# Optimization experiments

Measured on AMD Instinct MI355X. Metric: run time of the kernel, lower is better.

Reference implementation:

```python
import jax, jax.numpy as jnp
import numpy as np
from jax import lax

EPS = 1e-5
K_UP = 5
RATIO = 2
PAD = 2


def conv1x1(x, w):
    # x: (B,C,H,W), w: (O,C)
    return jnp.einsum('bchw,oc->bohw', x, w)


def bn(x, g, b, m, v):
    inv = g / jnp.sqrt(v + EPS)
    return x * inv[None, :, None, None] + (b - m * inv)[None, :, None, None]


def relu6(x):
    return jnp.clip(x, 0.0, 6.0)


def carafe_down(x, wc, bc, we, be):
    # content-aware reassembly kernels
    y = conv1x1(x, wc) + bc[None, :, None, None]              # (B, 64, H, W)
    y = lax.conv_general_dilated(
        y, we, window_strides=(RATIO, RATIO), padding=[(PAD, PAD), (PAD, PAD)],
        dimension_numbers=('NCHW', 'OIHW', 'NCHW')) + be[None, :, None, None]
    w = jax.nn.softmax(y, axis=1)                              # (B, 25, Ho, Wo)
    B, C, H, W = x.shape
    Ho, Wo = H // RATIO, W // RATIO
    xp = jnp.pad(x, ((0, 0), (0, 0), (PAD, PAD), (PAD, PAD)))
    out = jnp.zeros((B, C, Ho, Wo), x.dtype)
    k = 0
    for i in range(K_UP):
        for j in range(K_UP):
            patch = xp[:, :, i:i + RATIO * Ho:RATIO, j:j + RATIO * Wo:RATIO]
            out = out + patch * w[:, k][:, None]
            k += 1
    return out


def setup_inputs() -> dict:
    key = jax.random.key(0)
    ks = jax.random.split(key, 20)
    B, INP, H, W = 8, 64, 112, 112
    OUP, HID, CMID = 128, 384, 64

    def bn_params(k, c):
        k1, k2, k3, k4 = jax.random.split(k, 4)
        return (jax.random.uniform(k1, (c,), jnp.float32, 0.5, 1.5),
                jax.random.normal(k2, (c,), jnp.float32) * 0.1,
                jax.random.normal(k3, (c,), jnp.float32) * 0.1,
                jax.random.uniform(k4, (c,), jnp.float32, 0.5, 1.5))
    g1, b1, m1, v1 = bn_params(ks[1], HID)
    g2, b2, m2, v2 = bn_params(ks[2], HID)
    g3, b3, m3, v3 = bn_params(ks[3], OUP)
    return {
        'x': jax.random.normal(ks[0], (B, INP, H, W), jnp.float32),
        'w1': jax.random.normal(ks[4], (HID, INP), jnp.float32) / np.sqrt(INP),
        'g1': g1, 'b1': b1, 'm1': m1, 'v1': v1,
        'wc': jax.random.normal(ks[5], (CMID, HID), jnp.float32) / np.sqrt(HID),
        'bc': jax.random.normal(ks[6], (CMID,), jnp.float32) * 0.01,
        'we': jax.random.normal(ks[7], (K_UP**2, CMID, 5, 5), jnp.float32) / np.sqrt(CMID * 25),
        'be': jax.random.normal(ks[8], (K_UP**2,), jnp.float32) * 0.01,
        'g2': g2, 'b2': b2, 'm2': m2, 'v2': v2,
        'w2': jax.random.normal(ks[9], (OUP, HID), jnp.float32) / np.sqrt(HID),
        'g3': g3, 'b3': b3, 'm3': m3, 'v3': v3,
    }


def reference(x, w1, g1, b1, m1, v1, wc, bc, we, be, g2, b2, m2, v2, w2, g3, b3, m3, v3):
    # stride-2 InvertedResidualBlockCarafe (no identity): 1x1 expand -> BN -> ReLU6
    # -> CARAFE_downsample -> BN -> ReLU6 -> 1x1 project -> BN
    h = relu6(bn(conv1x1(x, w1), g1, b1, m1, v1))
    h = relu6(bn(carafe_down(h, wc, bc, we, be), g2, b2, m2, v2))
    return bn(conv1x1(h, w2), g3, b3, m3, v3)
```

## Files before the change

### kernel.cpp

```cpp
#include <hip/hip_runtime.h>
#include <hip/hip_bf16.h>
#include <type_traits>

#define EPS 1e-5f

typedef _Float16 half8 __attribute__((ext_vector_type(8)));
typedef _Float16 half4 __attribute__((ext_vector_type(4)));
typedef _Float16 half2v __attribute__((ext_vector_type(2)));
typedef float f32x4 __attribute__((ext_vector_type(4)));

__global__ __launch_bounds__(256) void fold_k(
    const float* __restrict__ w1, const float* __restrict__ g1, const float* __restrict__ b1,
    const float* __restrict__ m1, const float* __restrict__ v1,
    const float* __restrict__ wc,
    const float* __restrict__ g2, const float* __restrict__ b2,
    const float* __restrict__ m2, const float* __restrict__ v2,
    const float* __restrict__ w2, const float* __restrict__ g3, const float* __restrict__ b3,
    const float* __restrict__ m3, const float* __restrict__ v3,
    _Float16* __restrict__ w1h, float* __restrict__ bias1,
    _Float16* __restrict__ wch,
    _Float16* __restrict__ w2h, float* __restrict__ bias3,
    float* __restrict__ s2, float* __restrict__ t2) {
  int i = blockIdx.x * 256 + threadIdx.x;
  if (i < 384 * 64) {
    int o = i >> 6;
    float inv = g1[o] / sqrtf(v1[o] + EPS);
    w1h[i] = (_Float16)(w1[i] * inv);
  }
  if (i < 64 * 384) wch[i] = (_Float16)wc[i];
  if (i < 128 * 384) {
    int o = i / 384;
    float inv = g3[o] / sqrtf(v3[o] + EPS);
    w2h[i] = (_Float16)(w2[i] * inv);
  }
  if (i < 384) {
    float inv = g1[i] / sqrtf(v1[i] + EPS);
    bias1[i] = b1[i] - m1[i] * inv;
    float inv2 = g2[i] / sqrtf(v2[i] + EPS);
    s2[i] = inv2;
    t2[i] = b2[i] - m2[i] * inv2;
  }
  if (i < 128) {
    float inv = g3[i] / sqrtf(v3[i] + EPS);
    bias3[i] = b3[i] - m3[i] * inv;
  }
}

__global__ __launch_bounds__(256) void wtrans2_k(const float* __restrict__ we,
                                                 _Float16* __restrict__ wa) {
  int i = blockIdx.x * 256 + threadIdx.x;
  if (i >= 51200) return;
  int j = i & 7;
  int lane = (i >> 3) & 63;
  int f = i >> 9;
  int ocf = f & 1;
  int tap = (f >> 1) % 25;
  int ph = f / 50;
  int oc = ocf * 16 + (lane & 15);
  int cm = ph * 32 + (lane >> 4) * 8 + j;
  float v = (oc < 25) ? we[((size_t)oc * 64 + cm) * 25 + tap] : 0.f;
  wa[i] = (_Float16)v;
}

template <int IC, int NPF, int ACT, typename TI, typename TO>
__global__ __launch_bounds__(256) void gemm16_k(
    const TI* __restrict__ in, const _Float16* __restrict__ wh,
    const float* __restrict__ bias, TO* __restrict__ out, int npx) {
  constexpr int BPX = NPF * 64;
  constexpr int L2B = (BPX == 128) ? 7 : 6;
  constexpr int PAD = 16 / sizeof(TO);
  constexpr int CH = 16 / sizeof(TO);
  constexpr int SPAN = NPF * 16;
  constexpr int LPO = SPAN / CH;
  constexpr int OCPI = 64 / LPO;
  using vec16 = std::conditional_t<std::is_same_v<TO, _Float16>, half8, float4>;

  __shared__ _Float16 xh[BPX][40];
  __shared__ TO oT[64][BPX + PAD];

  const int tid = threadIdx.x;
  const int lane = tid & 63;
  const int w = tid >> 6;
  const int l15 = lane & 15;
  const int g = lane >> 4;
  const int wpx = w * SPAN;
  const int oc0 = blockIdx.x * 64;
  const int p0 = blockIdx.y * BPX;
  const int b = blockIdx.z;
  const int OCT = gridDim.x * 64;
  const TI* inb = in + (size_t)b * IC * npx + p0;

  f32x4 acc[4][NPF];
#pragma unroll
  for (int fo = 0; fo < 4; ++fo)
#pragma unroll
    for (int pf = 0; pf < NPF; ++pf)
      acc[fo][pf] = (f32x4){0.f, 0.f, 0.f, 0.f};

  for (int kk = 0; kk < IC; kk += 32) {
    __syncthreads();
    half8 a[4];
#pragma unroll
    for (int fo = 0; fo < 4; ++fo)
      a[fo] = *(const half8*)&wh[(size_t)(oc0 + fo * 16 + l15) * IC + kk + g * 8];
#pragma unroll
    for (int i = 0; i < NPF * 2; ++i) {
      int slot = tid + 256 * i;
      int px = slot & (BPX - 1);
      int kq = slot >> L2B;
      const TI* src = inb + (size_t)(kk + kq * 4) * npx + px;
      half4 v = {(_Float16)src[0], (_Float16)src[npx],
                 (_Float16)src[2 * npx], (_Float16)src[3 * npx]};
      *(half4*)&xh[px][kq * 4] = v;
    }
    __syncthreads();
    half8 xb[NPF];
#pragma unroll
    for (int pf = 0; pf < NPF; ++pf)
      xb[pf] = *(const half8*)&xh[wpx + pf * 16 + l15][g * 8];
#pragma unroll
    for (int fo = 0; fo < 4; ++fo)
#pragma unroll
      for (int pf = 0; pf < NPF; ++pf)
        acc[fo][pf] = __builtin_amdgcn_mfma_f32_16x16x32_f16(
            a[fo], xb[pf], acc[fo][pf], 0, 0, 0);
  }

#pragma unroll
  for (int fo = 0; fo < 4; ++fo) {
#pragma unroll
    for (int r = 0; r < 4; ++r) {
      float bz = bias[oc0 + fo * 16 + g * 4 + r];
#pragma unroll
      for (int pf = 0; pf < NPF; ++pf) {
        float v = acc[fo][pf][r] + bz;
        if (ACT) v = fminf(fmaxf(v, 0.f), 6.f);
        oT[fo * 16 + g * 4 + r][wpx + pf * 16 + l15] = (TO)v;
      }
    }
  }
#pragma unroll
  for (int i = 0; i < LPO; ++i) {
    int oc = i * OCPI + lane / LPO;
    int pxo = (lane % LPO) * CH;
    vec16 v = *(const vec16*)&oT[oc][wpx + pxo];
    *(vec16*)&out[((size_t)b * OCT + oc0 + oc) * npx + p0 + wpx + pxo] = v;
  }
}

__global__ __launch_bounds__(256) void mask_conv5_k(
    const _Float16* __restrict__ y, const _Float16* __restrict__ wa,
    float* __restrict__ lg) {
  __shared__ _Float16 ysh[32][5][136];
  const int ho = blockIdx.x;
  const int b = blockIdx.y;
  const int tid = threadIdx.x;
  const int lane = tid & 63;
  const int w = tid >> 6;
  const int l15 = lane & 15;
  const int g = lane >> 4;
  const int wo = w * 16 + l15;
  const int woe = (wo < 56) ? wo : 55;
  const int ci0 = 2 * woe + 6;

  for (int i = tid; i < 640; i += 256) {
    int ch = i / 20; int rem = i - ch * 20; int ri = rem / 4; int q = rem & 3;
    *(uint*)&ysh[ch][ri][q * 2] = 0u;
  }
  for (int i = tid; i < 1280; i += 256) {
    int ch = i / 40; int rem = i - ch * 40; int ri = rem / 8; int q = rem & 7;
    *(uint*)&ysh[ch][ri][120 + q * 2] = 0u;
  }

  f32x4 acc[2] = {(f32x4){0.f, 0.f, 0.f, 0.f}, (f32x4){0.f, 0.f, 0.f, 0.f}};

  for (int ph = 0; ph < 2; ++ph) {
    __syncthreads();
    for (int i = tid; i < 2240; i += 256) {
      int ch = i / 70;
      int rem = i - ch * 70;
      int ri = rem / 14;
      int j8 = rem - ri * 14;
      int hi = 2 * ho - 2 + ri;
      half8 v = {0, 0, 0, 0, 0, 0, 0, 0};
      if ((unsigned)hi < 112u)
        v = *(const half8*)&y[((size_t)(b * 64 + ph * 32 + ch) * 112 + hi) * 112 + j8 * 8];
      *(half8*)&ysh[ch][ri][8 + j8 * 8] = v;
    }
    __syncthreads();

    const _Float16* wap = wa + (size_t)ph * 25600;
#pragma unroll
    for (int di = 0; di < 5; ++di) {
      half2v pa[8], pb[8];
      _Float16 pc[8];
#pragma unroll
      for (int j = 0; j < 8; ++j) {
        pa[j] = *(const half2v*)&ysh[g * 8 + j][di][ci0];
        pb[j] = *(const half2v*)&ysh[g * 8 + j][di][ci0 + 2];
        pc[j] = ysh[g * 8 + j][di][ci0 + 4];
      }
#pragma unroll
      for (int dj = 0; dj < 5; ++dj) {
        half8 bf;
#pragma unroll
        for (int j = 0; j < 8; ++j)
          bf[j] = (dj == 0) ? pa[j][0]
                : (dj == 1) ? pa[j][1]
                : (dj == 2) ? pb[j][0]
                : (dj == 3) ? pb[j][1]
                            : pc[j];
        const int tap = di * 5 + dj;
        half8 a0 = *(const half8*)&wap[(tap * 2 + 0) * 512 + lane * 8];
        half8 a1 = *(const half8*)&wap[(tap * 2 + 1) * 512 + lane * 8];
        acc[0] = __builtin_amdgcn_mfma_f32_16x16x32_f16(a0, bf, acc[0], 0, 0, 0);
        acc[1] = __builtin_amdgcn_mfma_f32_16x16x32_f16(a1, bf, acc[1], 0, 0, 0);
      }
    }
  }

  if (wo < 56) {
#pragma unroll
    for (int ocf = 0; ocf < 2; ++ocf)
#pragma unroll
      for (int r = 0; r < 4; ++r) {
        int oc = ocf * 16 + g * 4 + r;
        if (oc < 25)
          lg[((size_t)b * 25 + oc) * 3136 + ho * 56 + wo] = acc[ocf][r];
      }
  }
}

__global__ __launch_bounds__(256) void softmax3_k(
    const float* __restrict__ lg, const float* __restrict__ be,
    float* __restrict__ msk) {
  int idx = blockIdx.x * 256 + threadIdx.x;
  if (idx >= 8 * 3136) return;
  int b = idx / 3136, sp = idx - (idx / 3136) * 3136;
  float v[25];
  float mx = -1e30f;
#pragma unroll
  for (int k = 0; k < 25; ++k) {
    float s = lg[((size_t)b * 25 + k) * 3136 + sp] + be[k];
    v[k] = s;
    mx = fmaxf(mx, s);
  }
  float s = 0.f;
#pragma unroll
  for (int k = 0; k < 25; ++k) {
    v[k] = __expf(v[k] - mx);
    s += v[k];
  }
  float inv = 1.0f / s;
#pragma unroll
  for (int k = 0; k < 25; ++k)
    msk[((size_t)b * 25 + k) * 3136 + sp] = v[k] * inv;
}

__device__ __forceinline__ void stage_pair(float dst[2][19][120],
                                           const _Float16* __restrict__ hbase,
                                           int ho0, int tid) {
  for (int i = tid; i < 2 * 19 * 14; i += 512) {
    int ch = i / 266;
    int rem = i - ch * 266;
    int rr = rem / 14;
    int j8 = rem - rr * 14;
    int hi = 2 * ho0 - 2 + rr;
    float4 lo = {0.f, 0.f, 0.f, 0.f}, hi4 = {0.f, 0.f, 0.f, 0.f};
    if ((unsigned)hi < 112u) {
      half8 v = *(const half8*)&hbase[(size_t)ch * 12544 + hi * 112 + j8 * 8];
      lo = (float4){(float)v[0], (float)v[1], (float)v[2], (float)v[3]};
      hi4 = (float4){(float)v[4], (float)v[5], (float)v[6], (float)v[7]};
    }
    *(float4*)&dst[ch][rr][4 + j8 * 8] = lo;
    *(float4*)&dst[ch][rr][8 + j8 * 8] = hi4;
  }
}

__global__ __launch_bounds__(512) void carafe3_k(
    const _Float16* __restrict__ h, const float* __restrict__ msk,
    const float* __restrict__ s2, const float* __restrict__ t2,
    _Float16* __restrict__ h2) {
  __shared__ float ys[2][2][19][120];
  const int hx = blockIdx.x;
  const int b  = blockIdx.y;
  const int cz = blockIdx.z;
  const int ho0 = hx * 8;
  const int tid = threadIdx.x;
  const int r = tid / 56;
  const int c = tid - r * 56;
  const int c0 = cz * 24;

  for (int i = tid; i < 2 * 2 * 19 * 8; i += 512) {
    int bufi = i / 304;
    int rem = i - bufi * 304;
    int ch = rem / 152;
    int rem2 = rem - ch * 152;
    int rr = rem2 / 8;
    int p = rem2 - rr * 8;
    int col = (p < 4) ? p : (112 + p);
    ys[bufi][ch][rr][col] = 0.f;
  }

  float m[25];
  if (tid < 448) {
    const float* mp = msk + (size_t)b * 25 * 3136 + (ho0 + r) * 56 + c;
#pragma unroll
    for (int k = 0; k < 25; ++k) m[k] = mp[(size_t)k * 3136];
  }
  __syncthreads();

  stage_pair(ys[0], h + (size_t)(b * 384 + c0) * 12544, ho0, tid);
  __syncthreads();

#pragma unroll
  for (int p = 0; p < 12; ++p) {
    const int bf = p & 1;
    if (p + 1 < 12)
      stage_pair(ys[bf ^ 1], h + (size_t)(b * 384 + c0 + 2 * (p + 1)) * 12544,
                 ho0, tid);
    if (tid < 448) {
#pragma unroll
      for (int cl = 0; cl < 2; ++cl) {
        const int cc = c0 + 2 * p + cl;
        float acc = 0.f;
#pragma unroll
        for (int di = 0; di < 5; ++di) {
          const float* row = &ys[bf][cl][2 * r + di][2 * c + 2];
          float2 a01 = *(const float2*)&row[0];
          float2 a23 = *(const float2*)&row[2];
          float a4 = row[4];
          acc = fmaf(a01.x, m[di * 5 + 0], acc);
          acc = fmaf(a01.y, m[di * 5 + 1], acc);
          acc = fmaf(a23.x, m[di * 5 + 2], acc);
          acc = fmaf(a23.y, m[di * 5 + 3], acc);
          acc = fmaf(a4,    m[di * 5 + 4], acc);
        }
        float o = s2[cc] * acc + t2[cc];
        h2[((size_t)(b * 384 + cc) * 56 + ho0 + r) * 56 + c] =
            (_Float16)fminf(fmaxf(o, 0.f), 6.f);
      }
    }
    __syncthreads();
  }
}

extern "C" void kernel_launch(void* const* d_in, const int* in_sizes, int n_in,
                              void* d_out, int out_size, void* d_ws, size_t ws_size,
                              hipStream_t stream) {
  const float* x  = (const float*)d_in[0];
  const float* w1 = (const float*)d_in[1];
  const float* g1 = (const float*)d_in[2];
  const float* b1 = (const float*)d_in[3];
  const float* m1 = (const float*)d_in[4];
  const float* v1 = (const float*)d_in[5];
  const float* wc = (const float*)d_in[6];
  const float* bc = (const float*)d_in[7];
  const float* we = (const float*)d_in[8];
  const float* be = (const float*)d_in[9];
  const float* g2 = (const float*)d_in[10];
  const float* b2 = (const float*)d_in[11];
  const float* m2 = (const float*)d_in[12];
  const float* v2 = (const float*)d_in[13];
  const float* w2 = (const float*)d_in[14];
  const float* g3 = (const float*)d_in[15];
  const float* b3 = (const float*)d_in[16];
  const float* m3 = (const float*)d_in[17];
  const float* v3 = (const float*)d_in[18];
  float* out = (float*)d_out;

  _Float16* hq  = (_Float16*)d_ws;
  _Float16* yq  = hq + 38535168;
  _Float16* h2q = yq + 6422528;
  float* lg     = (float*)(h2q + 9633792);
  float* mskf   = lg + 627200;
  float* bias1  = mskf + 627200;
  float* bias3  = bias1 + 384;
  float* s2     = bias3 + 128;
  float* t2     = s2 + 384;
  _Float16* w1h = (_Float16*)(t2 + 384);
  _Float16* wch = w1h + 24576;
  _Float16* w2h = wch + 24576;
  _Float16* wa  = w2h + 49152;

  fold_k<<<192, 256, 0, stream>>>(w1, g1, b1, m1, v1, wc, g2, b2, m2, v2,
                                  w2, g3, b3, m3, v3,
                                  w1h, bias1, wch, w2h, bias3, s2, t2);
  wtrans2_k<<<200, 256, 0, stream>>>(we, wa);

  gemm16_k<64, 2, 1, float, _Float16>
      <<<dim3(6, 98, 8), 256, 0, stream>>>(x, w1h, bias1, hq, 12544);

  gemm16_k<384, 2, 0, _Float16, _Float16>
      <<<dim3(1, 98, 8), 256, 0, stream>>>(hq, wch, bc, yq, 12544);

  mask_conv5_k<<<dim3(56, 8), 256, 0, stream>>>(yq, wa, lg);
  softmax3_k<<<98, 256, 0, stream>>>(lg, be, mskf);

  carafe3_k<<<dim3(7, 8, 16), 512, 0, stream>>>(hq, mskf, s2, t2, h2q);

  gemm16_k<384, 1, 0, _Float16, float>
      <<<dim3(2, 49, 8), 256, 0, stream>>>(h2q, w2h, bias3, out, 3136);
}
```

Baseline: 162.5 us.

## Fuse expand GEMM and CARAFE compressor GEMM into one kernel

Adds a fused kernel that computes the 1x1 expand conv with BN and ReLU6 for all 384 channels of a 64-pixel tile, keeps the result in shared memory, and feeds it straight into the 384-to-64 compressor GEMM. The separate re-read of the 384-channel fp16 intermediate from global memory for the second GEMM goes away. The intermediate is still written out for the later CARAFE stage. The kernel uses about 62KB of LDS and 96 accumulator VGPRs per thread, which may limit occupancy. The grid axes of the generic GEMM are also swapped so that pixel tiles come first.

```diff
diff --git a/kernel.cpp b/kernel.cpp
--- a/kernel.cpp
+++ b/kernel.cpp
@@ -62,6 +62,105 @@
   wa[i] = (_Float16)v;
 }
 
+__global__ __launch_bounds__(256) void fused1_k(
+    const float* __restrict__ x, const _Float16* __restrict__ w1h,
+    const float* __restrict__ bias1, const _Float16* __restrict__ wch,
+    const float* __restrict__ bc, _Float16* __restrict__ hq,
+    _Float16* __restrict__ yq) {
+  __shared__ __align__(16) unsigned char smem_raw[63488];
+  _Float16 (*xh)[40]  = (_Float16 (*)[40])smem_raw;
+  _Float16 (*hT)[76]  = (_Float16 (*)[76])(smem_raw + 5120);
+  _Float16 (*oTy)[72] = (_Float16 (*)[72])(smem_raw + 5120);
+
+  const int tid = threadIdx.x;
+  const int lane = tid & 63;
+  const int w = tid >> 6;
+  const int l15 = lane & 15;
+  const int g = lane >> 4;
+  const int wpx = w * 16;
+  const int p0 = blockIdx.x * 64;
+  const int b = blockIdx.y;
+  const float* inb = x + (size_t)b * 64 * 12544 + p0;
+
+  f32x4 acc1[24];
+#pragma unroll
+  for (int fo = 0; fo < 24; ++fo) acc1[fo] = (f32x4){0.f, 0.f, 0.f, 0.f};
+
+  for (int kk = 0; kk < 64; kk += 32) {
+    __syncthreads();
+#pragma unroll
+    for (int i = 0; i < 2; ++i) {
+      int slot = tid + 256 * i;
+      int px = slot & 63;
+      int kq = slot >> 6;
+      const float* src = inb + (size_t)(kk + kq * 4) * 12544 + px;
+      half4 v = {(_Float16)src[0], (_Float16)src[12544],
+                 (_Float16)src[2 * 12544], (_Float16)src[3 * 12544]};
+      *(half4*)&xh[px][kq * 4] = v;
+    }
+    __syncthreads();
+    half8 xb = *(const half8*)&xh[wpx + l15][g * 8];
+#pragma unroll
+    for (int fo = 0; fo < 24; ++fo) {
+      half8 a = *(const half8*)&w1h[(size_t)(fo * 16 + l15) * 64 + kk + g * 8];
+      acc1[fo] = __builtin_amdgcn_mfma_f32_16x16x32_f16(a, xb, acc1[fo], 0, 0, 0);
+    }
+  }
+
+#pragma unroll
+  for (int fo = 0; fo < 24; ++fo) {
+#pragma unroll
+    for (int r = 0; r < 4; ++r) {
+      int oc = fo * 16 + g * 4 + r;
+      float v = acc1[fo][r] + bias1[oc];
+      v = fminf(fmaxf(v, 0.f), 6.f);
+      hT[oc][wpx + l15] = (_Float16)v;
+    }
+  }
+  __syncthreads();
+
+#pragma unroll
+  for (int i = 0; i < 12; ++i) {
+    int idx = tid + 256 * i;
+    int row = idx >> 3, j8 = idx & 7;
+    half8 v = *(const half8*)&hT[row][j8 * 8];
+    *(half8*)&hq[(size_t)(b * 384 + row) * 12544 + p0 + j8 * 8] = v;
+  }
+
+  f32x4 acc2[4];
+#pragma unroll
+  for (int fo2 = 0; fo2 < 4; ++fo2) acc2[fo2] = (f32x4){0.f, 0.f, 0.f, 0.f};
+#pragma unroll
+  for (int ks = 0; ks < 12; ++ks) {
+    half8 bf;
+#pragma unroll
+    for (int j = 0; j < 8; ++j) bf[j] = hT[ks * 32 + g * 8 + j][wpx + l15];
+#pragma unroll
+    for (int fo2 = 0; fo2 < 4; ++fo2) {
+      half8 a = *(const half8*)&wch[(size_t)(fo2 * 16 + l15) * 384 + ks * 32 + g * 8];
+      acc2[fo2] = __builtin_amdgcn_mfma_f32_16x16x32_f16(a, bf, acc2[fo2], 0, 0, 0);
+    }
+  }
+  __syncthreads();
+
+#pragma unroll
+  for (int fo2 = 0; fo2 < 4; ++fo2) {
+#pragma unroll
+    for (int r = 0; r < 4; ++r) {
+      int oc2 = fo2 * 16 + g * 4 + r;
+      oTy[oc2][wpx + l15] = (_Float16)(acc2[fo2][r] + bc[oc2]);
+    }
+  }
+  __syncthreads();
+#pragma unroll
+  for (int i = 0; i < 2; ++i) {
+    int slot = tid + 256 * i;
+    int row = slot >> 3, j8 = slot & 7;
+    half8 v = *(const half8*)&oTy[row][j8 * 8];
+    *(half8*)&yq[(size_t)(b * 64 + row) * 12544 + p0 + j8 * 8] = v;
+  }
+}
+
 template <int IC, int NPF, int ACT, typename TI, typename TO>
 __global__ __launch_bounds__(256) void gemm16_k(
     const TI* __restrict__ in, const _Float16* __restrict__ wh,
@@ -84,10 +183,10 @@
   const int l15 = lane & 15;
   const int g = lane >> 4;
   const int wpx = w * SPAN;
-  const int oc0 = blockIdx.x * 64;
-  const int p0 = blockIdx.y * BPX;
+  const int p0 = blockIdx.x * BPX;
+  const int oc0 = blockIdx.y * 64;
   const int b = blockIdx.z;
-  const int OCT = gridDim.x * 64;
+  const int OCT = gridDim.y * 64;
   const TI* inb = in + (size_t)b * IC * npx + p0;
 
   f32x4 acc[4][NPF];
@@ -388,11 +487,7 @@
                                   w1h, bias1, wch, w2h, bias3, s2, t2);
   wtrans2_k<<<200, 256, 0, stream>>>(we, wa);
 
-  gemm16_k<64, 2, 1, float, _Float16>
-      <<<dim3(6, 98, 8), 256, 0, stream>>>(x, w1h, bias1, hq, 12544);
-
-  gemm16_k<384, 2, 0, _Float16, _Float16>
-      <<<dim3(1, 98, 8), 256, 0, stream>>>(hq, wch, bc, yq, 12544);
+  fused1_k<<<dim3(196, 8), 256, 0, stream>>>(x, w1h, bias1, wch, bc, hq, yq);
 
   mask_conv5_k<<<dim3(56, 8), 256, 0, stream>>>(yq, wa, lg);
   softmax3_k<<<98, 256, 0, stream>>>(lg, be, mskf);
@@ -400,5 +495,5 @@
   carafe3_k<<<dim3(7, 8, 16), 512, 0, stream>>>(hq, mskf, s2, t2, h2q);
 
   gemm16_k<384, 1, 0, _Float16, float>
-      <<<dim3(2, 49, 8), 256, 0, stream>>>(h2q, w2h, bias3, out, 3136);
-}
+      <<<dim3(49, 2, 8), 256, 0, stream>>>(h2q, w2h, bias3, out, 3136);
+}
```

Result: slower. 181.6 us (+11.8%).

## Fuse softmax into mask conv and remap GEMM blocks for XCD locality

Applied to the files above, without the earlier changes.

The softmax over the 25 reassembly logits now runs inside the mask convolution kernel. Logits are staged in shared memory and normalized by 56 threads, which removes a separate launch and the global round trip of the logit tensor. The GEMM kernels switch to a 1D grid whose block index is decoded so that blocks sharing a pixel tile and batch land on the same XCD (wg&7) and reuse input through L2. The softmax now uses few threads per block, and the mapping assumes 8 XCDs with round-robin dispatch.

```diff
diff --git a/kernel.cpp b/kernel.cpp
--- a/kernel.cpp
+++ b/kernel.cpp
@@ -62,7 +62,7 @@
   wa[i] = (_Float16)v;
 }
 
-template <int IC, int NPF, int ACT, typename TI, typename TO>
+template <int IC, int NPF, int ACT, int NOC, int NPXT, typename TI, typename TO>
 __global__ __launch_bounds__(256) void gemm16_k(
     const TI* __restrict__ in, const _Float16* __restrict__ wh,
     const float* __restrict__ bias, TO* __restrict__ out, int npx) {
@@ -84,10 +84,19 @@
   const int l15 = lane & 15;
   const int g = lane >> 4;
   const int wpx = w * SPAN;
-  const int oc0 = blockIdx.x * 64;
-  const int p0 = blockIdx.y * BPX;
-  const int b = blockIdx.z;
-  const int OCT = gridDim.x * 64;
+
+  const int wg = blockIdx.x;
+  const int xcd = wg & 7;
+  const int s = wg >> 3;
+  const int oct = s % NOC;
+  const int gl = s / NOC;
+  const int grp = gl * 8 + xcd;
+  const int pxt = grp % NPXT;
+  const int b = grp / NPXT;
+
+  const int p0 = pxt * BPX;
+  const int oc0 = oct * 64;
+  const int OCT = NOC * 64;
   const TI* inb = in + (size_t)b * IC * npx + p0;
 
   f32x4 acc[4][NPF];
@@ -148,10 +157,11 @@
   }
 }
 
-__global__ __launch_bounds__(256) void mask_conv5_k(
+__global__ __launch_bounds__(256) void mask_conv6_k(
     const _Float16* __restrict__ y, const _Float16* __restrict__ wa,
-    float* __restrict__ lg) {
+    const float* __restrict__ be, float* __restrict__ msk) {
   __shared__ _Float16 ysh[32][5][136];
+  __shared__ float lsm[32][66];
   const int ho = blockIdx.x;
   const int b = blockIdx.y;
   const int tid = threadIdx.x;
@@ -219,42 +229,33 @@
     }
   }
 
-  if (wo < 56) {
-#pragma unroll
-    for (int ocf = 0; ocf < 2; ++ocf)
-#pragma unroll
-      for (int r = 0; r < 4; ++r) {
-        int oc = ocf * 16 + g * 4 + r;
-        if (oc < 25)
-          lg[((size_t)b * 25 + oc) * 3136 + ho * 56 + wo] = acc[ocf][r];
-      }
-  }
-}
-
-__global__ __launch_bounds__(256) void softmax3_k(
-    const float* __restrict__ lg, const float* __restrict__ be,
-    float* __restrict__ msk) {
-  int idx = blockIdx.x * 256 + threadIdx.x;
-  if (idx >= 8 * 3136) return;
-  int b = idx / 3136, sp = idx - (idx / 3136) * 3136;
-  float v[25];
-  float mx = -1e30f;
-#pragma unroll
-  for (int k = 0; k < 25; ++k) {
-    float s = lg[((size_t)b * 25 + k) * 3136 + sp] + be[k];
-    v[k] = s;
-    mx = fmaxf(mx, s);
-  }
-  float s = 0.f;
-#pragma unroll
-  for (int k = 0; k < 25; ++k) {
-    v[k] = __expf(v[k] - mx);
-    s += v[k];
-  }
-  float inv = 1.0f / s;
-#pragma unroll
-  for (int k = 0; k < 25; ++k)
-    msk[((size_t)b * 25 + k) * 3136 + sp] = v[k] * inv;
+#pragma unroll
+  for (int ocf = 0; ocf < 2; ++ocf)
+#pragma unroll
+    for (int r = 0; r < 4; ++r)
+      lsm[ocf * 16 + g * 4 + r][w * 16 + l15] = acc[ocf][r];
+  __syncthreads();
+
+  if (tid < 56) {
+    float v[25];
+    float mx = -1e30f;
+#pragma unroll
+    for (int k = 0; k < 25; ++k) {
+      float s = lsm[k][tid] + be[k];
+      v[k] = s;
+      mx = fmaxf(mx, s);
+    }
+    float s = 0.f;
+#pragma unroll
+    for (int k = 0; k < 25; ++k) {
+      v[k] = __expf(v[k] - mx);
+      s += v[k];
+    }
+    float inv = 1.0f / s;
+#pragma unroll
+    for (int k = 0; k < 25; ++k)
+      msk[((size_t)b * 25 + k) * 3136 + ho * 56 + tid] = v[k] * inv;
+  }
 }
 
 __device__ __forceinline__ void stage_pair(float dst[2][19][120],
@@ -372,8 +373,7 @@
   _Float16* hq  = (_Float16*)d_ws;
   _Float16* yq  = hq + 38535168;
   _Float16* h2q = yq + 6422528;
-  float* lg     = (float*)(h2q + 9633792);
-  float* mskf   = lg + 627200;
+  float* mskf   = (float*)(h2q + 9633792);
   float* bias1  = mskf + 627200;
   float* bias3  = bias1 + 384;
   float* s2     = bias3 + 128;
@@ -388,17 +388,16 @@
                                   w1h, bias1, wch, w2h, bias3, s2, t2);
   wtrans2_k<<<200, 256, 0, stream>>>(we, wa);
 
-  gemm16_k<64, 2, 1, float, _Float16>
-      <<<dim3(6, 98, 8), 256, 0, stream>>>(x, w1h, bias1, hq, 12544);
-
-  gemm16_k<384, 2, 0, _Float16, _Float16>
-      <<<dim3(1, 98, 8), 256, 0, stream>>>(hq, wch, bc, yq, 12544);
-
-  mask_conv5_k<<<dim3(56, 8), 256, 0, stream>>>(yq, wa, lg);
-  softmax3_k<<<98, 256, 0, stream>>>(lg, be, mskf);
+  gemm16_k<64, 2, 1, 6, 98, float, _Float16>
+      <<<6 * 98 * 8, 256, 0, stream>>>(x, w1h, bias1, hq, 12544);
+
+  gemm16_k<384, 2, 0, 1, 98, _Float16, _Float16>
+      <<<1 * 98 * 8, 256, 0, stream>>>(hq, wch, bc, yq, 12544);
+
+  mask_conv6_k<<<dim3(56, 8), 256, 0, stream>>>(yq, wa, be, mskf);
 
   carafe3_k<<<dim3(7, 8, 16), 512, 0, stream>>>(hq, mskf, s2, t2, h2q);
 
-  gemm16_k<384, 1, 0, _Float16, float>
-      <<<dim3(2, 49, 8), 256, 0, stream>>>(h2q, w2h, bias3, out, 3136);
-}
+  gemm16_k<384, 1, 0, 2, 49, _Float16, float>
+      <<<2 * 49 * 8, 256, 0, stream>>>(h2q, w2h, bias3, out, 3136);
+}
```

Result: faster. 156.3 us (-3.8%).
